# Kernel tuning notes

Hardware: AMD Instinct MI355X
Metric: run time of the kernel (lower is better)

## Reference

```python
import jax, jax.numpy as jnp
import numpy as np

IN_DIMS = 32
HID = 64
N_HIDDEN = 5  # tcnn n_hidden_layers = hidden_layers + 1 = 5
OUT_DIMS = 3
BATCH = 2097152


def setup_inputs() -> dict:
    key = jax.random.key(0)
    ks = jax.random.split(key, N_HIDDEN + 2)
    x = jax.random.normal(ks[0], (BATCH, IN_DIMS), dtype=jnp.float32)
    # tcnn FullyFusedMLP has no biases; Kaiming-ish init scale
    W0 = jax.random.normal(ks[1], (IN_DIMS, HID), dtype=jnp.float32) * (1.0 / np.sqrt(IN_DIMS))
    Wh = jax.random.normal(ks[2], (N_HIDDEN - 1, HID, HID), dtype=jnp.float32) * (1.0 / np.sqrt(HID))
    Wo = jax.random.normal(ks[3], (HID, OUT_DIMS), dtype=jnp.float32) * (1.0 / np.sqrt(HID))
    return {"x": x, "W0": W0, "Wh": Wh, "Wo": Wo}


def reference(x, W0, Wh, Wo):
    # input layer -> ReLU
    h = jax.nn.relu(x @ W0)  # [B, 64]
    # 4 more hidden layers of 64->64 with ReLU (small fixed count, unrolled)
    for i in range(Wh.shape[0]):
        h = jax.nn.relu(h @ Wh[i])
    # linear output layer (output_activation = None)
    return h @ Wo  # [B, 3]
```

## Files before the change

kernel.cpp:

```cpp
#include <hip/hip_runtime.h>


typedef __attribute__((ext_vector_type(8))) short short8;
typedef __attribute__((ext_vector_type(4))) float f32x4;

#define BATCH   2097152
#define NBLOCKS 2048
#define ROWS    64
#define ITERS   (BATCH / (NBLOCKS * ROWS))
static_assert(BATCH % (NBLOCKS * ROWS) == 0, "");

__device__ __forceinline__ short f2bf_rne(float f) {
    unsigned u = __builtin_bit_cast(unsigned, f);
    u += 0x7FFFu + ((u >> 16) & 1u);
    return (short)(u >> 16);
}

__device__ __forceinline__ unsigned pack2(float a, float b) {
    unsigned ua = __builtin_bit_cast(unsigned, a) + 0x8000u;
    unsigned ub = __builtin_bit_cast(unsigned, b) + 0x8000u;
    return __builtin_amdgcn_perm(ub, ua, 0x07060302u);
}

__global__ __launch_bounds__(256, 4)
void mlp_fused(const float* __restrict__ x, const float* __restrict__ W0,
               const float* __restrict__ Wh, const float* __restrict__ Wo,
               float* __restrict__ out)
{
    __shared__ __align__(16) unsigned char smem[2][ROWS * 128];

    const int tid  = threadIdx.x;
    const int w    = tid >> 6;
    const int lane = tid & 63;
    const int n = lane & 15;
    const int q = lane >> 4;

    short8 wf0, wfh[4][2], wfo[2];
    {
        const float* p = W0 + (8 * q) * 64 + 16 * w + n;
        short8 f;
        #pragma unroll
        for (int j = 0; j < 8; ++j) f[j] = f2bf_rne(p[j * 64]);
        wf0 = f;
    }
    #pragma unroll
    for (int l = 0; l < 4; ++l) {
        #pragma unroll
        for (int c = 0; c < 2; ++c) {
            const float* p = Wh + l * 4096 + (32 * c + 8 * q) * 64 + 16 * w + n;
            short8 f;
            #pragma unroll
            for (int j = 0; j < 8; ++j) f[j] = f2bf_rne(p[j * 64]);
            wfh[l][c] = f;
        }
    }
    #pragma unroll
    for (int c = 0; c < 2; ++c) {
        short8 f;
        #pragma unroll
        for (int j = 0; j < 8; ++j)
            f[j] = (n < 3) ? f2bf_rne(Wo[(32 * c + 8 * q + j) * 3 + n]) : (short)0;
        wfo[c] = f;
    }

    const int m7 = n & 7;
    const unsigned wbase = (unsigned)n * 128u
                         + 16u * (unsigned)((2 * w + (q >> 1)) ^ m7)
                         + 8u * (unsigned)(q & 1);
    const unsigned r0 = (unsigned)n * 128u + 16u * (unsigned)((q) ^ m7);
    const unsigned r1 = (unsigned)n * 128u + 16u * (unsigned)((4 + q) ^ m7);

    const f32x4 z = {0.f, 0.f, 0.f, 0.f};
    f32x4 xa[4][2];

    auto load_x = [&](int it) {
        const size_t base = ((size_t)it * NBLOCKS + blockIdx.x) * ROWS;
        #pragma unroll
        for (int j = 0; j < 4; ++j) {
            const f32x4* xp = (const f32x4*)(x + (base + 16 * j + n) * 32) + 2 * q;
            xa[j][0] = xp[0];
            xa[j][1] = xp[1];
        }
    };

    load_x(0);

    for (int it = 0; it < ITERS; ++it) {
        const size_t base = ((size_t)it * NBLOCKS + blockIdx.x) * ROWS;

        f32x4 acc[4];
        #pragma unroll
        for (int j = 0; j < 4; ++j) {
            union { unsigned u[4]; short8 s; } bin;
            bin.u[0] = pack2(xa[j][0][0], xa[j][0][1]);
            bin.u[1] = pack2(xa[j][0][2], xa[j][0][3]);
            bin.u[2] = pack2(xa[j][1][0], xa[j][1][1]);
            bin.u[3] = pack2(xa[j][1][2], xa[j][1][3]);
            acc[j] = __builtin_amdgcn_mfma_f32_16x16x32_bf16(wf0, bin.s, z, 0, 0, 0);
        }

        #pragma unroll
        for (int s = 0; s < 5; ++s) {
            unsigned char* buf = smem[s & 1];

            #pragma unroll
            for (int j = 0; j < 4; ++j) {
                uint2 wv;
                wv.x = pack2(fmaxf(acc[j][0], 0.f), fmaxf(acc[j][1], 0.f));
                wv.y = pack2(fmaxf(acc[j][2], 0.f), fmaxf(acc[j][3], 0.f));
                *(uint2*)(buf + wbase + j * 2048) = wv;
            }

            if (s == 4 && it + 1 < ITERS) load_x(it + 1);

            __syncthreads();

            if (s < 4) {
                short8 b0[4], b1[4];
                #pragma unroll
                for (int j = 0; j < 4; ++j)
                    b0[j] = *(const short8*)(buf + r0 + j * 2048);
                #pragma unroll
                for (int j = 0; j < 4; ++j)
                    b1[j] = *(const short8*)(buf + r1 + j * 2048);
                #pragma unroll
                for (int j = 0; j < 4; ++j)
                    acc[j] = __builtin_amdgcn_mfma_f32_16x16x32_bf16(
                                 wfh[s][0], b0[j], z, 0, 0, 0);
                #pragma unroll
                for (int j = 0; j < 4; ++j)
                    acc[j] = __builtin_amdgcn_mfma_f32_16x16x32_bf16(
                                 wfh[s][1], b1[j], acc[j], 0, 0, 0);
            } else {
                short8 c0 = *(const short8*)(buf + r0 + w * 2048);
                short8 c1 = *(const short8*)(buf + r1 + w * 2048);
                f32x4 o = __builtin_amdgcn_mfma_f32_16x16x32_bf16(wfo[0], c0, z, 0, 0, 0);
                o = __builtin_amdgcn_mfma_f32_16x16x32_bf16(wfo[1], c1, o, 0, 0, 0);
                if (lane < 16) {
                    float* po = out + (base + 16 * w + lane) * 3;
                    po[0] = o[0];
                    po[1] = o[1];
                    po[2] = o[2];
                }
            }
        }
        __syncthreads();
    }
}

extern "C" void kernel_launch(void* const* d_in, const int* in_sizes, int n_in,
                              void* d_out, int out_size, void* d_ws, size_t ws_size,
                              hipStream_t stream) {
    (void)in_sizes; (void)n_in; (void)d_ws; (void)ws_size; (void)out_size;
    const float* x  = (const float*)d_in[0];
    const float* W0 = (const float*)d_in[1];
    const float* Wh = (const float*)d_in[2];
    const float* Wo = (const float*)d_in[3];
    float* out = (float*)d_out;
    mlp_fused<<<NBLOCKS, 256, 0, stream>>>(x, W0, Wh, Wo, out);
}
```

Measured before the change: 443.3 us.

## Give each wave its own rows and full weights to drop block barriers

Restructures the fused MLP so each wave handles its own 16-row tile and keeps every output-column slice of all weight matrices in registers. The hidden activation is exchanged only inside the wave through a private padded LDS region, which removes all __syncthreads. The grid is halved and occupancy is lowered to 2 blocks per CU. Next-tile x is prefetched and converted to bf16 early, and the manual bf16 rounding is replaced with v_cvt_pk_bf16_f32. The cost is much higher register pressure from holding roughly four times the weight fragments, and it relies on wave-level ordering of LDS writes and reads with no explicit barrier.

```diff
diff --git a/kernel.cpp b/kernel.cpp
--- a/kernel.cpp
+++ b/kernel.cpp
@@ -5,29 +5,26 @@
 typedef __attribute__((ext_vector_type(4))) float f32x4;
 
 #define BATCH   2097152
-#define NBLOCKS 2048
-#define ROWS    64
-#define ITERS   (BATCH / (NBLOCKS * ROWS))
-static_assert(BATCH % (NBLOCKS * ROWS) == 0, "");
+#define NBLOCKS 1024
+#define WAVES   (NBLOCKS * 4)
+#define ITERS   (BATCH / (WAVES * 16))
+#define RSTRIDE 144
+#define BUFSZ   (16 * RSTRIDE)
+#define WREGION (2 * BUFSZ)
+static_assert(BATCH == NBLOCKS * 4 * 16 * ITERS, "");
 
-__device__ __forceinline__ short f2bf_rne(float f) {
-    unsigned u = __builtin_bit_cast(unsigned, f);
-    u += 0x7FFFu + ((u >> 16) & 1u);
-    return (short)(u >> 16);
+__device__ __forceinline__ unsigned cvt_pk(float a, float b) {
+    unsigned r;
+    asm("v_cvt_pk_bf16_f32 %0, %1, %2" : "=v"(r) : "v"(a), "v"(b));
+    return r;
 }
 
-__device__ __forceinline__ unsigned pack2(float a, float b) {
-    unsigned ua = __builtin_bit_cast(unsigned, a) + 0x8000u;
-    unsigned ub = __builtin_bit_cast(unsigned, b) + 0x8000u;
-    return __builtin_amdgcn_perm(ub, ua, 0x07060302u);
-}
-
-__global__ __launch_bounds__(256, 4)
+__global__ __launch_bounds__(256, 2)
 void mlp_fused(const float* __restrict__ x, const float* __restrict__ W0,
                const float* __restrict__ Wh, const float* __restrict__ Wo,
                float* __restrict__ out)
 {
-    __shared__ __align__(16) unsigned char smem[2][ROWS * 128];
+    __shared__ __align__(16) unsigned char smem[4 * WREGION];
 
     const int tid  = threadIdx.x;
     const int w    = tid >> 6;
@@ -35,116 +32,117 @@
     const int n = lane & 15;
     const int q = lane >> 4;
 
-    short8 wf0, wfh[4][2], wfo[2];
-    {
-        const float* p = W0 + (8 * q) * 64 + 16 * w + n;
-        short8 f;
+    short8 wf0[4], wfh[4][4][2], wfo[2];
+    #pragma unroll
+    for (int t = 0; t < 4; ++t) {
+        const float* p = W0 + (8 * q) * 64 + 16 * t + n;
+        union { unsigned u[4]; short8 s; } f;
         #pragma unroll
-        for (int j = 0; j < 8; ++j) f[j] = f2bf_rne(p[j * 64]);
-        wf0 = f;
+        for (int i = 0; i < 4; ++i)
+            f.u[i] = cvt_pk(p[(2 * i) * 64], p[(2 * i + 1) * 64]);
+        wf0[t] = f.s;
     }
     #pragma unroll
-    for (int l = 0; l < 4; ++l) {
+    for (int l = 0; l < 4; ++l)
         #pragma unroll
-        for (int c = 0; c < 2; ++c) {
-            const float* p = Wh + l * 4096 + (32 * c + 8 * q) * 64 + 16 * w + n;
-            short8 f;
+        for (int t = 0; t < 4; ++t)
             #pragma unroll
-            for (int j = 0; j < 8; ++j) f[j] = f2bf_rne(p[j * 64]);
-            wfh[l][c] = f;
-        }
-    }
+            for (int c = 0; c < 2; ++c) {
+                const float* p = Wh + l * 4096 + (32 * c + 8 * q) * 64 + 16 * t + n;
+                union { unsigned u[4]; short8 s; } f;
+                #pragma unroll
+                for (int i = 0; i < 4; ++i)
+                    f.u[i] = cvt_pk(p[(2 * i) * 64], p[(2 * i + 1) * 64]);
+                wfh[l][t][c] = f.s;
+            }
     #pragma unroll
     for (int c = 0; c < 2; ++c) {
-        short8 f;
+        union { unsigned u[4]; short8 s; } f;
         #pragma unroll
-        for (int j = 0; j < 8; ++j)
-            f[j] = (n < 3) ? f2bf_rne(Wo[(32 * c + 8 * q + j) * 3 + n]) : (short)0;
-        wfo[c] = f;
+        for (int i = 0; i < 4; ++i) {
+            float a = (n < 3) ? Wo[(32 * c + 8 * q + 2 * i)     * 3 + n] : 0.f;
+            float b = (n < 3) ? Wo[(32 * c + 8 * q + 2 * i + 1) * 3 + n] : 0.f;
+            f.u[i] = cvt_pk(a, b);
+        }
+        wfo[c] = f.s;
     }
 
-    const int m7 = n & 7;
-    const unsigned wbase = (unsigned)n * 128u
-                         + 16u * (unsigned)((2 * w + (q >> 1)) ^ m7)
-                         + 8u * (unsigned)(q & 1);
-    const unsigned r0 = (unsigned)n * 128u + 16u * (unsigned)((q) ^ m7);
-    const unsigned r1 = (unsigned)n * 128u + 16u * (unsigned)((4 + q) ^ m7);
+    unsigned char* const smw = smem + w * WREGION;
+    const unsigned aw = (unsigned)n * RSTRIDE + 8u  * (unsigned)q;
+    const unsigned ar = (unsigned)n * RSTRIDE + 16u * (unsigned)q;
 
+    const int gw = blockIdx.x * 4 + w;
     const f32x4 z = {0.f, 0.f, 0.f, 0.f};
-    f32x4 xa[4][2];
 
-    auto load_x = [&](int it) {
-        const size_t base = ((size_t)it * NBLOCKS + blockIdx.x) * ROWS;
-        #pragma unroll
-        for (int j = 0; j < 4; ++j) {
-            const f32x4* xp = (const f32x4*)(x + (base + 16 * j + n) * 32) + 2 * q;
-            xa[j][0] = xp[0];
-            xa[j][1] = xp[1];
-        }
-    };
+    short8 xfn;
+    {
+        const f32x4* xp = (const f32x4*)(x + ((size_t)gw * 16 + n) * 32) + 2 * q;
+        f32x4 a = xp[0], b = xp[1];
+        union { unsigned u[4]; short8 s; } f;
+        f.u[0] = cvt_pk(a[0], a[1]); f.u[1] = cvt_pk(a[2], a[3]);
+        f.u[2] = cvt_pk(b[0], b[1]); f.u[3] = cvt_pk(b[2], b[3]);
+        xfn = f.s;
+    }
 
-    load_x(0);
-
+    #pragma unroll 1
     for (int it = 0; it < ITERS; ++it) {
-        const size_t base = ((size_t)it * NBLOCKS + blockIdx.x) * ROWS;
+        const short8 xf   = xfn;
+        const size_t row0 = ((size_t)it * WAVES + gw) * 16;
 
         f32x4 acc[4];
         #pragma unroll
-        for (int j = 0; j < 4; ++j) {
-            union { unsigned u[4]; short8 s; } bin;
-            bin.u[0] = pack2(xa[j][0][0], xa[j][0][1]);
-            bin.u[1] = pack2(xa[j][0][2], xa[j][0][3]);
-            bin.u[2] = pack2(xa[j][1][0], xa[j][1][1]);
-            bin.u[3] = pack2(xa[j][1][2], xa[j][1][3]);
-            acc[j] = __builtin_amdgcn_mfma_f32_16x16x32_bf16(wf0, bin.s, z, 0, 0, 0);
+        for (int t = 0; t < 4; ++t)
+            acc[t] = __builtin_amdgcn_mfma_f32_16x16x32_bf16(wf0[t], xf, z, 0, 0, 0);
+
+        if (it + 1 < ITERS) {
+            const size_t r1 = ((size_t)(it + 1) * WAVES + gw) * 16;
+            const f32x4* xp = (const f32x4*)(x + (r1 + n) * 32) + 2 * q;
+            f32x4 a = xp[0], b = xp[1];
+            union { unsigned u[4]; short8 s; } f;
+            f.u[0] = cvt_pk(a[0], a[1]); f.u[1] = cvt_pk(a[2], a[3]);
+            f.u[2] = cvt_pk(b[0], b[1]); f.u[3] = cvt_pk(b[2], b[3]);
+            xfn = f.s;
         }
 
         #pragma unroll
         for (int s = 0; s < 5; ++s) {
-            unsigned char* buf = smem[s & 1];
+            unsigned char* buf = smw + (((unsigned)(s + it) & 1u) * BUFSZ);
 
             #pragma unroll
-            for (int j = 0; j < 4; ++j) {
+            for (int t = 0; t < 2; ++t) {
                 uint2 wv;
-                wv.x = pack2(fmaxf(acc[j][0], 0.f), fmaxf(acc[j][1], 0.f));
-                wv.y = pack2(fmaxf(acc[j][2], 0.f), fmaxf(acc[j][3], 0.f));
-                *(uint2*)(buf + wbase + j * 2048) = wv;
+                wv.x = cvt_pk(fmaxf(acc[t][0], 0.f), fmaxf(acc[t][1], 0.f));
+                wv.y = cvt_pk(fmaxf(acc[t][2], 0.f), fmaxf(acc[t][3], 0.f));
+                *(uint2*)(buf + aw + 32u * t) = wv;
             }
-
-            if (s == 4 && it + 1 < ITERS) load_x(it + 1);
-
-            __syncthreads();
+            short8 b0 = *(const short8*)(buf + ar);
+            #pragma unroll
+            for (int t = 2; t < 4; ++t) {
+                uint2 wv;
+                wv.x = cvt_pk(fmaxf(acc[t][0], 0.f), fmaxf(acc[t][1], 0.f));
+                wv.y = cvt_pk(fmaxf(acc[t][2], 0.f), fmaxf(acc[t][3], 0.f));
+                *(uint2*)(buf + aw + 32u * t) = wv;
+            }
+            short8 b1 = *(const short8*)(buf + ar + 64u);
 
             if (s < 4) {
-                short8 b0[4], b1[4];
                 #pragma unroll
-                for (int j = 0; j < 4; ++j)
-                    b0[j] = *(const short8*)(buf + r0 + j * 2048);
+                for (int t = 0; t < 4; ++t)
+                    acc[t] = __builtin_amdgcn_mfma_f32_16x16x32_bf16(
+                                 wfh[s][t][0], b0, z, 0, 0, 0);
                 #pragma unroll
-                for (int j = 0; j < 4; ++j)
-                    b1[j] = *(const short8*)(buf + r1 + j * 2048);
-                #pragma unroll
-                for (int j = 0; j < 4; ++j)
-                    acc[j] = __builtin_amdgcn_mfma_f32_16x16x32_bf16(
-                                 wfh[s][0], b0[j], z, 0, 0, 0);
-                #pragma unroll
-                for (int j = 0; j < 4; ++j)
-                    acc[j] = __builtin_amdgcn_mfma_f32_16x16x32_bf16(
-                                 wfh[s][1], b1[j], acc[j], 0, 0, 0);
+                for (int t = 0; t < 4; ++t)
+                    acc[t] = __builtin_amdgcn_mfma_f32_16x16x32_bf16(
+                                 wfh[s][t][1], b1, acc[t], 0, 0, 0);
             } else {
-                short8 c0 = *(const short8*)(buf + r0 + w * 2048);
-                short8 c1 = *(const short8*)(buf + r1 + w * 2048);
-                f32x4 o = __builtin_amdgcn_mfma_f32_16x16x32_bf16(wfo[0], c0, z, 0, 0, 0);
-                o = __builtin_amdgcn_mfma_f32_16x16x32_bf16(wfo[1], c1, o, 0, 0, 0);
+                f32x4 o = __builtin_amdgcn_mfma_f32_16x16x32_bf16(wfo[0], b0, z, 0, 0, 0);
+                o = __builtin_amdgcn_mfma_f32_16x16x32_bf16(wfo[1], b1, o, 0, 0, 0);
                 if (lane < 16) {
-                    float* po = out + (base + 16 * w + lane) * 3;
-                    po[0] = o[0];
-                    po[1] = o[1];
-                    po[2] = o[2];
+                    float* po = out + (row0 + lane) * 3;
+                    po[0] = o[0]; po[1] = o[1]; po[2] = o[2];
                 }
             }
         }
-        __syncthreads();
     }
 }
 
```

Measured after the change: 402.2 us. 9.3% less time.
